# Kernel optimization log

Hardware: AMD Instinct MI355X
Metric: run time of the kernel (lower is better)

## Reference

```python
import jax, jax.numpy as jnp
import numpy as np

HIDDEN = 2048
HEADS = 32
HEAD_DIM = HIDDEN // HEADS  # 64
MAX_POS = 512
TABLE = 2 * MAX_POS - 1  # 1023


def setup_inputs() -> dict:
    key = jax.random.key(0)
    k = jax.random.split(key, 6)
    B, S = 16, 512
    return {
        "hidden_states": jax.random.normal(k[0], (B, S, HIDDEN), dtype=jnp.float32),
        "wq": jax.random.normal(k[1], (HIDDEN, HIDDEN), dtype=jnp.float32) * 0.02,
        "wk": jax.random.normal(k[2], (HIDDEN, HIDDEN), dtype=jnp.float32) * 0.02,
        "wv": jax.random.normal(k[3], (HIDDEN, HIDDEN), dtype=jnp.float32) * 0.02,
        "wo": jax.random.normal(k[4], (HIDDEN, HIDDEN), dtype=jnp.float32) * 0.02,
        "rel_pos": jax.random.normal(k[5], (TABLE, HEAD_DIM), dtype=jnp.float32),
    }


def _rel_bias(rel_pos, seq_len):
    pos = jnp.arange(seq_len)
    rel = pos[None, :] - pos[:, None] + (MAX_POS - 1)  # [S, S]
    rel = jnp.clip(rel, 0, TABLE - 1)
    return rel_pos[rel].mean(axis=-1)  # [S, S]


def reference(hidden_states, wq, wk, wv, wo, rel_pos):
    B, S, _ = hidden_states.shape
    scale = jnp.sqrt(jnp.float32(HEAD_DIM))
    # nn.Linear(x) = x @ W.T
    q = (hidden_states @ wq.T).reshape(B, S, HEADS, HEAD_DIM).transpose(0, 2, 1, 3)
    k = (hidden_states @ wk.T).reshape(B, S, HEADS, HEAD_DIM).transpose(0, 2, 1, 3)
    v = (hidden_states @ wv.T).reshape(B, S, HEADS, HEAD_DIM).transpose(0, 2, 1, 3)
    scores = jnp.einsum("bhqd,bhkd->bhqk", q, k) / scale
    scores = scores + _rel_bias(rel_pos, S)[None, None]  # seq_len <= 512 path
    attn = jax.nn.softmax(scores, axis=-1)
    ctx = jnp.einsum("bhqk,bhkd->bhqd", attn, v)
    ctx = ctx.transpose(0, 2, 1, 3).reshape(B, S, HIDDEN)
    return ctx @ wo.T
```

## Files before the change

### kernel.cpp

```cpp
#include <hip/hip_runtime.h>

typedef __attribute__((ext_vector_type(8))) short bf16x8;
typedef __attribute__((ext_vector_type(4))) float f32x4;
typedef const __attribute__((address_space(3))) unsigned short* lds_cp;

#define DEVI __device__ __forceinline__

template <int N> struct IC { static constexpr int v = N; };

DEVI unsigned short f2bf(float f) {
  union { float f; unsigned u; } v; v.f = f;
  unsigned r = v.u + 0x7FFFu + ((v.u >> 16) & 1u);
  return (unsigned short)(r >> 16);
}

DEVI void gload16(const void* g, void* l) {
  __builtin_amdgcn_global_load_lds(
      (const __attribute__((address_space(1))) unsigned int*)g,
      (__attribute__((address_space(3))) unsigned int*)l, 16, 0, 0);
}

template <int OFF>
DEVI bf16x8 lreadT(lds_cp p) {
  bf16x8 r;
  asm volatile("ds_read_b128 %0, %1 offset:%2" : "=v"(r) : "v"(p), "i"(OFF));
  return r;
}

template <int OFF>
DEVI void read_af(lds_cp a0, lds_cp a1, bf16x8 (&f)[4][2]) {
  f[0][0] = lreadT<OFF + 0>(a0);    f[0][1] = lreadT<OFF + 0>(a1);
  f[1][0] = lreadT<OFF + 2048>(a0); f[1][1] = lreadT<OFF + 2048>(a1);
  f[2][0] = lreadT<OFF + 4096>(a0); f[2][1] = lreadT<OFF + 4096>(a1);
  f[3][0] = lreadT<OFF + 6144>(a0); f[3][1] = lreadT<OFF + 6144>(a1);
}
template <int OFF>
DEVI void read_bq(lds_cp b0, lds_cp b1, bf16x8 (&f)[2][2]) {
  f[0][0] = lreadT<OFF + 0>(b0);    f[0][1] = lreadT<OFF + 0>(b1);
  f[1][0] = lreadT<OFF + 2048>(b0); f[1][1] = lreadT<OFF + 2048>(b1);
}

#define MFMA16(a, b, c) __builtin_amdgcn_mfma_f32_16x16x32_bf16(a, b, c, 0, 0, 0)
#define LGKM(n) asm volatile("s_waitcnt lgkmcnt(" #n ")")
#define SBAR() __builtin_amdgcn_sched_barrier(0)

__global__ void cvt_kernel(const float* __restrict__ in,
                           unsigned short* __restrict__ out, int n4) {
  int i = blockIdx.x * blockDim.x + threadIdx.x;
  if (i < n4) {
    float4 v = ((const float4*)in)[i];
    ushort4 o;
    o.x = f2bf(v.x); o.y = f2bf(v.y); o.z = f2bf(v.z); o.w = f2bf(v.w);
    ((ushort4*)out)[i] = o;
  }
}

__global__ void cvt4_kernel(const float* __restrict__ a,
                            const float* __restrict__ b,
                            const float* __restrict__ c,
                            const float* __restrict__ d,
                            unsigned short* __restrict__ out) {
  int i = blockIdx.x * blockDim.x + threadIdx.x;
  const int w = i >> 20, l = i & 1048575;
  const float* s = (w == 0) ? a : (w == 1) ? b : (w == 2) ? c : d;
  float4 v = ((const float4*)s)[l];
  ushort4 o;
  o.x = f2bf(v.x); o.y = f2bf(v.y); o.z = f2bf(v.z); o.w = f2bf(v.w);
  ((ushort4*)out)[i] = o;
}

__global__ void bias_kernel(const float* __restrict__ rel_pos,
                            float* __restrict__ bias1d) {
  int t = blockIdx.x * blockDim.x + threadIdx.x;
  if (t < 1023) {
    const float* r = rel_pos + t * 64;
    float s = 0.f;
#pragma unroll
    for (int d = 0; d < 64; ++d) s += r[d];
    bias1d[t] = s * (1.44269504f / 64.0f);
  }
}

template <int MODE, int NT>
__global__ __launch_bounds__(512, 2) void gemm256(
    const unsigned short* __restrict__ A, const unsigned short* __restrict__ B,
    void* __restrict__ Cout, void* __restrict__ Cout2, void* __restrict__ Cout3) {
  __shared__ unsigned short As[2][16384];
  __shared__ unsigned short Bs[2][16384];

  const int tid = threadIdx.x;
  const int logical = (blockIdx.x & 7) * (4 * NT) + (blockIdx.x >> 3);
  const int nt = logical % NT, mt = logical / NT;
  const int m0 = mt * 256, n0 = nt * 256;
  const int lane = tid & 63, wid = tid >> 6;
  const int wr = wid >> 2, wc = wid & 3;
  const int g = lane >> 4, c = lane & 15;

  const int srow = tid >> 3, sj = (tid & 7) ^ (srow & 7);
  const unsigned short* pA0[2];
  const unsigned short* pB0[2];
  unsigned short* lA0[2];
  unsigned short* lB0[2];
#pragma unroll
  for (int ch = 0; ch < 2; ++ch) {
    const int row = ch * 64 + srow;
    pA0[ch] = A + (size_t)(m0 + row) * 2048u + sj * 8;
    pB0[ch] = B + (size_t)(n0 + row) * 2048u + sj * 8;
    const int slot = ch * 512 + tid;
    lA0[ch] = &As[0][slot * 8];
    lB0[ch] = &Bs[0][slot * 8];
  }

  const int rA = wr * 128 + c;
  const int rB = wc * 64 + c;
  lds_cp aA0 = (lds_cp)&As[0][rA * 64 + (((0 + g) ^ (rA & 7)) * 8)];
  lds_cp aA1 = (lds_cp)&As[0][rA * 64 + (((4 + g) ^ (rA & 7)) * 8)];
  lds_cp aB0 = (lds_cp)&Bs[0][rB * 64 + (((0 + g) ^ (rB & 7)) * 8)];
  lds_cp aB1 = (lds_cp)&Bs[0][rB * 64 + (((4 + g) ^ (rB & 7)) * 8)];

  f32x4 acc[8][4];
#pragma unroll
  for (int i = 0; i < 8; ++i)
#pragma unroll
    for (int j = 0; j < 4; ++j) acc[i][j] = (f32x4){0.f, 0.f, 0.f, 0.f};

  bf16x8 af[4][2], bq0[2][2], bq1[2][2];

#pragma unroll
  for (int ch = 0; ch < 2; ++ch) {
    gload16(pA0[ch], lA0[ch]);
    gload16(pA0[ch] + 262144, lA0[ch] + 8192);
    gload16(pB0[ch], lB0[ch]);
    gload16(pB0[ch] + 262144, lB0[ch] + 8192);
  }
#pragma unroll
  for (int ch = 0; ch < 2; ++ch) {
    gload16(pA0[ch] + 64, lA0[ch] + 16384);
    gload16(pA0[ch] + 262144 + 64, lA0[ch] + 8192 + 16384);
  }
  asm volatile("s_waitcnt vmcnt(4)" ::: "memory");
  SBAR();
  __builtin_amdgcn_s_barrier();

  auto ktile = [&](auto B_, auto SB_, auto SA_, auto LB_, auto LA_, int kt) {
    constexpr int BOFF = decltype(B_)::v;
    constexpr int SB = decltype(SB_)::v;
    constexpr int SA = decltype(SA_)::v;
    constexpr int LB = decltype(LB_)::v;
    constexpr int LA = decltype(LA_)::v;

    read_bq<BOFF>(aB0, aB1, bq0);
    read_af<BOFF>(aA0, aA1, af);
    read_bq<BOFF + 4096>(aB0, aB1, bq1);
    if (kt + 1 < 32) {
      gload16(pB0[0] + SB, lB0[0] + LB);
      gload16(pB0[1] + SB, lB0[1] + LB);
      gload16(pB0[0] + 262144 + SB, lB0[0] + 8192 + LB);
      gload16(pB0[1] + 262144 + SB, lB0[1] + 8192 + LB);
    }
    LGKM(12);
    __builtin_amdgcn_s_barrier();
    LGKM(4);
    SBAR();
    __builtin_amdgcn_s_setprio(1);
#pragma unroll
    for (int kk = 0; kk < 2; ++kk)
#pragma unroll
      for (int mi = 0; mi < 4; ++mi)
#pragma unroll
        for (int ni = 0; ni < 2; ++ni)
          acc[mi][ni] = MFMA16(af[mi][kk], bq0[ni][kk], acc[mi][ni]);
    __builtin_amdgcn_s_setprio(0);
    LGKM(0);
    SBAR();
    __builtin_amdgcn_s_setprio(1);
#pragma unroll
    for (int kk = 0; kk < 2; ++kk)
#pragma unroll
      for (int mi = 0; mi < 4; ++mi)
#pragma unroll
        for (int ni = 0; ni < 2; ++ni)
          acc[mi][ni + 2] = MFMA16(af[mi][kk], bq1[ni][kk], acc[mi][ni + 2]);
    __builtin_amdgcn_s_setprio(0);
    __builtin_amdgcn_s_barrier();

    read_af<BOFF + 8192>(aA0, aA1, af);
    LGKM(4);
    __builtin_amdgcn_s_barrier();
    LGKM(0);
    SBAR();
    if (kt + 2 < 32) {
      gload16(pA0[0] + SA, lA0[0] + LA);
      gload16(pA0[1] + SA, lA0[1] + LA);
      gload16(pA0[0] + 262144 + SA, lA0[0] + 8192 + LA);
      gload16(pA0[1] + 262144 + SA, lA0[1] + 8192 + LA);
    }
    __builtin_amdgcn_s_setprio(1);
#pragma unroll
    for (int kk = 0; kk < 2; ++kk)
#pragma unroll
      for (int mi = 0; mi < 4; ++mi)
#pragma unroll
        for (int ni = 0; ni < 2; ++ni)
          acc[mi + 4][ni] = MFMA16(af[mi][kk], bq0[ni][kk], acc[mi + 4][ni]);
#pragma unroll
    for (int kk = 0; kk < 2; ++kk)
#pragma unroll
      for (int mi = 0; mi < 4; ++mi)
#pragma unroll
        for (int ni = 0; ni < 2; ++ni)
          acc[mi + 4][ni + 2] = MFMA16(af[mi][kk], bq1[ni][kk], acc[mi + 4][ni + 2]);
    __builtin_amdgcn_s_setprio(0);
    if (kt < 30) {
      asm volatile("s_waitcnt vmcnt(4)" ::: "memory");
    } else {
      asm volatile("s_waitcnt vmcnt(0)" ::: "memory");
    }
    SBAR();
    __builtin_amdgcn_s_barrier();
  };

  for (int t2 = 0; t2 < 16; ++t2) {
    ktile(IC<0>{}, IC<64>{}, IC<128>{}, IC<16384>{}, IC<0>{}, 2 * t2);
    ktile(IC<32768>{}, IC<128>{}, IC<192>{}, IC<0>{}, IC<16384>{}, 2 * t2 + 1);
#pragma unroll
    for (int ch = 0; ch < 2; ++ch) { pA0[ch] += 128; pB0[ch] += 128; }
  }

  const int rbase = m0 + wr * 128 + g * 4;
  const int cbase = n0 + wc * 64 + c;
  if (MODE == 0) {
    float* O = (float*)Cout;
#pragma unroll
    for (int mi = 0; mi < 8; ++mi)
#pragma unroll
      for (int ni = 0; ni < 4; ++ni)
#pragma unroll
        for (int rr = 0; rr < 4; ++rr)
          O[(size_t)(rbase + mi * 16 + rr) * 2048u + (cbase + ni * 16)] =
              acc[mi][ni][rr];
  } else {
    const int qsel = cbase >> 11;
    if (qsel < 2) {
      unsigned short* O = (unsigned short*)(qsel == 0 ? Cout : Cout2);
#pragma unroll
      for (int mi = 0; mi < 8; ++mi)
#pragma unroll
        for (int ni = 0; ni < 4; ++ni)
#pragma unroll
          for (int rr = 0; rr < 4; ++rr)
            O[(size_t)(rbase + mi * 16 + rr) * 2048u +
              ((cbase + ni * 16) & 2047)] = f2bf(acc[mi][ni][rr]);
    } else {
      unsigned short* O = (unsigned short*)Cout3;
#pragma unroll
      for (int mi = 0; mi < 8; ++mi)
#pragma unroll
        for (int ni = 0; ni < 4; ++ni) {
          const int row = rbase + mi * 16;
          const int col = (cbase + ni * 16) & 2047;
          const int bq_ = row >> 9, s = row & 511;
          const int hh = col >> 6, dd = col & 63;
          ushort4 o;
          o.x = f2bf(acc[mi][ni][0]);
          o.y = f2bf(acc[mi][ni][1]);
          o.z = f2bf(acc[mi][ni][2]);
          o.w = f2bf(acc[mi][ni][3]);
          *(ushort4*)(O + ((size_t)((bq_ * 32 + hh) * 64 + dd) << 9) + s) = o;
        }
    }
  }
}

__global__ __launch_bounds__(256, 3) void attn_kernel(
    const unsigned short* __restrict__ Q, const unsigned short* __restrict__ K,
    const unsigned short* __restrict__ VT, const float* __restrict__ bias1d,
    unsigned short* __restrict__ CTX) {
  __shared__ unsigned short Ksh[2][4096];
  __shared__ unsigned short Vsh[2][4096];
  __shared__ unsigned short Pb[4][2048];
  __shared__ float bl[1024];

  const int tid = threadIdx.x;
  const int wave = tid >> 6;
  const int lane = tid & 63;
  const int g = lane >> 4, c = lane & 15;

  const int logical = (blockIdx.x & 7) * 256 + (blockIdx.x >> 3);
  const int qc = logical & 3;
  const int bh = logical >> 2;
  const int b = bh >> 5, h = bh & 31;
  const int qrow0 = qc * 128 + wave * 32;

  for (int i = tid; i < 1023; i += 256) bl[i] = bias1d[i];

  bf16x8 aq[2][2];
  {
    const unsigned short* qb =
        Q + (size_t)(b * 512 + qrow0 + c) * 2048u + h * 64 + g * 8;
#pragma unroll
    for (int mi = 0; mi < 2; ++mi)
#pragma unroll
      for (int kk = 0; kk < 2; ++kk)
        aq[mi][kk] = *(const bf16x8*)(qb + mi * 16 * 2048 + kk * 32);
  }

  const unsigned short* kgb = K + (size_t)(b * 512) * 2048u + h * 64;
  const unsigned short* vgb = VT + (size_t)(bh * 64) * 512u;

  auto stage = [&](int buf, int kt) {
#pragma unroll
    for (int half = 0; half < 2; ++half) {
      const int slot = half * 256 + wave * 64 + lane;
      const int row = slot >> 3;
      const int j = (slot & 7) ^ (row & 7);
      gload16(kgb + (size_t)(kt * 64 + row) * 2048u + j * 8,
              &Ksh[buf][slot * 8]);
      gload16(vgb + (size_t)row * 512u + kt * 64 + j * 8, &Vsh[buf][slot * 8]);
    }
  };

  f32x4 o[2][4];
#pragma unroll
  for (int mi = 0; mi < 2; ++mi)
#pragma unroll
    for (int di = 0; di < 4; ++di) o[mi][di] = (f32x4){0.f, 0.f, 0.f, 0.f};
  float lreg[2][4];
#pragma unroll
  for (int mi = 0; mi < 2; ++mi)
#pragma unroll
    for (int rr = 0; rr < 4; ++rr) lreg[mi][rr] = 0.f;

  stage(0, 0);
  __syncthreads();

  const float SSCALE = 0.125f * 1.44269504f;

  for (int kt = 0; kt < 8; ++kt) {
    const int buf = kt & 1;
    if (kt < 7) stage(buf ^ 1, kt + 1);

    f32x4 s[2][4];
#pragma unroll
    for (int ni = 0; ni < 4; ++ni) {
      const unsigned short* kr = &Ksh[buf][(ni * 16 + c) * 64];
      bf16x8 bk0 = *(const bf16x8*)(kr + ((0 + g) ^ (c & 7)) * 8);
      bf16x8 bk1 = *(const bf16x8*)(kr + ((4 + g) ^ (c & 7)) * 8);
#pragma unroll
      for (int mi = 0; mi < 2; ++mi) {
        f32x4 z = (f32x4){0.f, 0.f, 0.f, 0.f};
        z = MFMA16(aq[mi][0], bk0, z);
        z = MFMA16(aq[mi][1], bk1, z);
        s[mi][ni] = z;
      }
    }

    unsigned short* pw = &Pb[wave][0];
#pragma unroll
    for (int mi = 0; mi < 2; ++mi)
#pragma unroll
      for (int rr = 0; rr < 4; ++rr) {
        const int prow = mi * 16 + g * 4 + rr;
        const int off0 = kt * 64 + c - (qrow0 + prow) + 511;
        float e0 = __builtin_amdgcn_exp2f(s[mi][0][rr] * SSCALE + bl[off0]);
        float e1 = __builtin_amdgcn_exp2f(s[mi][1][rr] * SSCALE + bl[off0 + 16]);
        float e2 = __builtin_amdgcn_exp2f(s[mi][2][rr] * SSCALE + bl[off0 + 32]);
        float e3 = __builtin_amdgcn_exp2f(s[mi][3][rr] * SSCALE + bl[off0 + 48]);
        lreg[mi][rr] += (e0 + e1) + (e2 + e3);
        const int rx = prow * 64, sw = (c >> 3) ^ (prow & 7), cl = c & 7;
        pw[rx + ((0 ^ sw) * 8 | cl)] = f2bf(e0);
        pw[rx + ((2 ^ sw) * 8 | cl)] = f2bf(e1);
        pw[rx + ((4 ^ sw) * 8 | cl)] = f2bf(e2);
        pw[rx + ((6 ^ sw) * 8 | cl)] = f2bf(e3);
      }

#pragma unroll
    for (int kk = 0; kk < 2; ++kk) {
      bf16x8 pa0 =
          *(const bf16x8*)(pw + (0 + c) * 64 + ((kk * 4 + g) ^ (c & 7)) * 8);
      bf16x8 pa1 =
          *(const bf16x8*)(pw + (16 + c) * 64 + ((kk * 4 + g) ^ (c & 7)) * 8);
#pragma unroll
      for (int di = 0; di < 4; ++di) {
        bf16x8 vb = *(const bf16x8*)(&Vsh[buf][(di * 16 + c) * 64 +
                                               ((kk * 4 + g) ^ (c & 7)) * 8]);
        o[0][di] = MFMA16(pa0, vb, o[0][di]);
        o[1][di] = MFMA16(pa1, vb, o[1][di]);
      }
    }
    __syncthreads();
  }

#pragma unroll
  for (int mi = 0; mi < 2; ++mi)
#pragma unroll
    for (int rr = 0; rr < 4; ++rr) {
      float l = lreg[mi][rr];
      l += __shfl_xor(l, 1);
      l += __shfl_xor(l, 2);
      l += __shfl_xor(l, 4);
      l += __shfl_xor(l, 8);
      const float rl = __builtin_amdgcn_rcpf(l);
      unsigned short* ob =
          CTX + (size_t)(b * 512 + qrow0 + mi * 16 + g * 4 + rr) * 2048u +
          h * 64 + c;
#pragma unroll
      for (int di = 0; di < 4; ++di) ob[di * 16] = f2bf(o[mi][di][rr] * rl);
    }
}

extern "C" void kernel_launch(void* const* d_in, const int* in_sizes, int n_in,
                              void* d_out, int out_size, void* d_ws,
                              size_t ws_size, hipStream_t stream) {
  const float* x = (const float*)d_in[0];
  const float* wq = (const float*)d_in[1];
  const float* wk = (const float*)d_in[2];
  const float* wv = (const float*)d_in[3];
  const float* wo = (const float*)d_in[4];
  const float* rel = (const float*)d_in[5];

  char* ws = (char*)d_ws;
  unsigned short* xb = (unsigned short*)(ws);
  unsigned short* wqb = (unsigned short*)(ws + 33554432);
  unsigned short* wob = wqb + 3 * 4194304;
  unsigned short* qb = (unsigned short*)(ws + 67108864);
  unsigned short* kb = qb + 16777216;
  unsigned short* vt = kb + 16777216;
  float* bias1 = (float*)(ws + 167772160);
  unsigned short* ctx = xb;

  cvt_kernel<<<16384, 256, 0, stream>>>(x, xb, 4194304);
  cvt4_kernel<<<16384, 256, 0, stream>>>(wq, wk, wv, wo, wqb);
  bias_kernel<<<4, 256, 0, stream>>>(rel, bias1);

  gemm256<3, 24><<<768, 512, 0, stream>>>(xb, wqb, qb, kb, vt);

  attn_kernel<<<2048, 256, 0, stream>>>(qb, kb, vt, bias1, ctx);

  gemm256<0, 8><<<256, 512, 0, stream>>>(ctx, wob, (float*)d_out, nullptr,
                                         nullptr);
}
```

Measured before the change: 340.2 us.

## Prefetch both A fragment halves and drop intra-tile barriers; fuse prep kernels

Reads both halves of the A fragments from LDS at the start of each k-tile into separate register sets. This lets two of the three workgroup barriers per k-tile be removed and overlaps LDS reads with MFMAs. It also merges the x conversion, weight conversion and bias reduction into a single launch to cut launch overhead. The extra fragment registers raise VGPR pressure, which could cause spills or lower occupancy.

```diff
diff --git a/kernel.cpp b/kernel.cpp
--- a/kernel.cpp
+++ b/kernel.cpp
@@ -44,40 +44,39 @@
 #define LGKM(n) asm volatile("s_waitcnt lgkmcnt(" #n ")")
 #define SBAR() __builtin_amdgcn_sched_barrier(0)
 
-__global__ void cvt_kernel(const float* __restrict__ in,
-                           unsigned short* __restrict__ out, int n4) {
-  int i = blockIdx.x * blockDim.x + threadIdx.x;
-  if (i < n4) {
-    float4 v = ((const float4*)in)[i];
+__global__ void prep_kernel(const float* __restrict__ x,
+                            const float* __restrict__ wq,
+                            const float* __restrict__ wk,
+                            const float* __restrict__ wv,
+                            const float* __restrict__ wo,
+                            const float* __restrict__ rel,
+                            unsigned short* __restrict__ xb,
+                            unsigned short* __restrict__ wqb,
+                            float* __restrict__ bias1) {
+  const int blk = blockIdx.x;
+  if (blk < 16384) {
+    const int i = blk * 256 + threadIdx.x;
+    float4 v = ((const float4*)x)[i];
     ushort4 o;
     o.x = f2bf(v.x); o.y = f2bf(v.y); o.z = f2bf(v.z); o.w = f2bf(v.w);
-    ((ushort4*)out)[i] = o;
-  }
-}
-
-__global__ void cvt4_kernel(const float* __restrict__ a,
-                            const float* __restrict__ b,
-                            const float* __restrict__ c,
-                            const float* __restrict__ d,
-                            unsigned short* __restrict__ out) {
-  int i = blockIdx.x * blockDim.x + threadIdx.x;
-  const int w = i >> 20, l = i & 1048575;
-  const float* s = (w == 0) ? a : (w == 1) ? b : (w == 2) ? c : d;
-  float4 v = ((const float4*)s)[l];
-  ushort4 o;
-  o.x = f2bf(v.x); o.y = f2bf(v.y); o.z = f2bf(v.z); o.w = f2bf(v.w);
-  ((ushort4*)out)[i] = o;
-}
-
-__global__ void bias_kernel(const float* __restrict__ rel_pos,
-                            float* __restrict__ bias1d) {
-  int t = blockIdx.x * blockDim.x + threadIdx.x;
-  if (t < 1023) {
-    const float* r = rel_pos + t * 64;
-    float s = 0.f;
-#pragma unroll
-    for (int d = 0; d < 64; ++d) s += r[d];
-    bias1d[t] = s * (1.44269504f / 64.0f);
+    ((ushort4*)xb)[i] = o;
+  } else if (blk < 32768) {
+    const int i = (blk - 16384) * 256 + threadIdx.x;
+    const int w = i >> 20, l = i & 1048575;
+    const float* s = (w == 0) ? wq : (w == 1) ? wk : (w == 2) ? wv : wo;
+    float4 v = ((const float4*)s)[l];
+    ushort4 o;
+    o.x = f2bf(v.x); o.y = f2bf(v.y); o.z = f2bf(v.z); o.w = f2bf(v.w);
+    ((ushort4*)wqb)[i] = o;
+  } else {
+    const int t = (blk - 32768) * 256 + threadIdx.x;
+    if (t < 1023) {
+      const float* r = rel + t * 64;
+      float s = 0.f;
+#pragma unroll
+      for (int d = 0; d < 64; ++d) s += r[d];
+      bias1[t] = s * (1.44269504f / 64.0f);
+    }
   }
 }
 
@@ -124,7 +123,7 @@
 #pragma unroll
     for (int j = 0; j < 4; ++j) acc[i][j] = (f32x4){0.f, 0.f, 0.f, 0.f};
 
-  bf16x8 af[4][2], bq0[2][2], bq1[2][2];
+  bf16x8 afl[4][2], afh[4][2], bq0[2][2], bq1[2][2];
 
 #pragma unroll
   for (int ch = 0; ch < 2; ++ch) {
@@ -150,17 +149,17 @@
     constexpr int LA = decltype(LA_)::v;
 
     read_bq<BOFF>(aB0, aB1, bq0);
-    read_af<BOFF>(aA0, aA1, af);
+    read_af<BOFF>(aA0, aA1, afl);
     read_bq<BOFF + 4096>(aB0, aB1, bq1);
+    read_af<BOFF + 8192>(aA0, aA1, afh);
     if (kt + 1 < 32) {
       gload16(pB0[0] + SB, lB0[0] + LB);
       gload16(pB0[1] + SB, lB0[1] + LB);
       gload16(pB0[0] + 262144 + SB, lB0[0] + 8192 + LB);
       gload16(pB0[1] + 262144 + SB, lB0[1] + 8192 + LB);
     }
+
     LGKM(12);
-    __builtin_amdgcn_s_barrier();
-    LGKM(4);
     SBAR();
     __builtin_amdgcn_s_setprio(1);
 #pragma unroll
@@ -169,32 +168,31 @@
       for (int mi = 0; mi < 4; ++mi)
 #pragma unroll
         for (int ni = 0; ni < 2; ++ni)
-          acc[mi][ni] = MFMA16(af[mi][kk], bq0[ni][kk], acc[mi][ni]);
+          acc[mi][ni] = MFMA16(afl[mi][kk], bq0[ni][kk], acc[mi][ni]);
     __builtin_amdgcn_s_setprio(0);
+
+    LGKM(8);
+    SBAR();
+    __builtin_amdgcn_s_setprio(1);
+#pragma unroll
+    for (int kk = 0; kk < 2; ++kk)
+#pragma unroll
+      for (int mi = 0; mi < 4; ++mi)
+#pragma unroll
+        for (int ni = 0; ni < 2; ++ni)
+          acc[mi][ni + 2] = MFMA16(afl[mi][kk], bq1[ni][kk], acc[mi][ni + 2]);
+    __builtin_amdgcn_s_setprio(0);
+
     LGKM(0);
     SBAR();
-    __builtin_amdgcn_s_setprio(1);
-#pragma unroll
-    for (int kk = 0; kk < 2; ++kk)
-#pragma unroll
-      for (int mi = 0; mi < 4; ++mi)
-#pragma unroll
-        for (int ni = 0; ni < 2; ++ni)
-          acc[mi][ni + 2] = MFMA16(af[mi][kk], bq1[ni][kk], acc[mi][ni + 2]);
-    __builtin_amdgcn_s_setprio(0);
     __builtin_amdgcn_s_barrier();
-
-    read_af<BOFF + 8192>(aA0, aA1, af);
-    LGKM(4);
-    __builtin_amdgcn_s_barrier();
-    LGKM(0);
-    SBAR();
     if (kt + 2 < 32) {
       gload16(pA0[0] + SA, lA0[0] + LA);
       gload16(pA0[1] + SA, lA0[1] + LA);
       gload16(pA0[0] + 262144 + SA, lA0[0] + 8192 + LA);
       gload16(pA0[1] + 262144 + SA, lA0[1] + 8192 + LA);
     }
+
     __builtin_amdgcn_s_setprio(1);
 #pragma unroll
     for (int kk = 0; kk < 2; ++kk)
@@ -202,15 +200,16 @@
       for (int mi = 0; mi < 4; ++mi)
 #pragma unroll
         for (int ni = 0; ni < 2; ++ni)
-          acc[mi + 4][ni] = MFMA16(af[mi][kk], bq0[ni][kk], acc[mi + 4][ni]);
+          acc[mi + 4][ni] = MFMA16(afh[mi][kk], bq0[ni][kk], acc[mi + 4][ni]);
 #pragma unroll
     for (int kk = 0; kk < 2; ++kk)
 #pragma unroll
       for (int mi = 0; mi < 4; ++mi)
 #pragma unroll
         for (int ni = 0; ni < 2; ++ni)
-          acc[mi + 4][ni + 2] = MFMA16(af[mi][kk], bq1[ni][kk], acc[mi + 4][ni + 2]);
+          acc[mi + 4][ni + 2] = MFMA16(afh[mi][kk], bq1[ni][kk], acc[mi + 4][ni + 2]);
     __builtin_amdgcn_s_setprio(0);
+
     if (kt < 30) {
       asm volatile("s_waitcnt vmcnt(4)" ::: "memory");
     } else {
@@ -429,9 +428,8 @@
   float* bias1 = (float*)(ws + 167772160);
   unsigned short* ctx = xb;
 
-  cvt_kernel<<<16384, 256, 0, stream>>>(x, xb, 4194304);
-  cvt4_kernel<<<16384, 256, 0, stream>>>(wq, wk, wv, wo, wqb);
-  bias_kernel<<<4, 256, 0, stream>>>(rel, bias1);
+  prep_kernel<<<32772, 256, 0, stream>>>(x, wq, wk, wv, wo, rel, xb, wqb,
+                                         bias1);
 
   gemm256<3, 24><<<768, 512, 0, stream>>>(xb, wqb, qb, kb, vt);
 
```

Result: no change. 334.0 us, median of 2 (-1.8%).
